# Performance work log

Measured on AMD Instinct MI355X. Metric: run time of the kernel, lower is better.

Reference implementation:

```python
import jax, jax.numpy as jnp
import numpy as np

COST_CLASS, COST_BBOX, COST_GIOU = 1.0, 5.0, 2.0  # init_kwargs weights


def cxcywh_to_xyxy(b):
    cx, cy, w, h = jnp.split(b, 4, axis=-1)
    return jnp.concatenate([cx - 0.5 * w, cy - 0.5 * h, cx + 0.5 * w, cy + 0.5 * h], axis=-1)


def generalized_box_iou(a, b):
    # a: [N,4], b: [M,4], xyxy. Returns [N,M] pairwise GIoU.
    area_a = (a[:, 2] - a[:, 0]) * (a[:, 3] - a[:, 1])
    area_b = (b[:, 2] - b[:, 0]) * (b[:, 3] - b[:, 1])
    lt = jnp.maximum(a[:, None, :2], b[None, :, :2])
    rb = jnp.minimum(a[:, None, 2:], b[None, :, 2:])
    wh = jnp.clip(rb - lt, 0.0)
    inter = wh[..., 0] * wh[..., 1]
    union = area_a[:, None] + area_b[None, :] - inter
    iou = inter / union
    lt_e = jnp.minimum(a[:, None, :2], b[None, :, :2])
    rb_e = jnp.maximum(a[:, None, 2:], b[None, :, 2:])
    wh_e = jnp.clip(rb_e - lt_e, 0.0)
    area_e = wh_e[..., 0] * wh_e[..., 1]
    return iou - (area_e - union) / area_e


def setup_inputs() -> dict:
    key = jax.random.key(0)
    k1, k2, k3, k4 = jax.random.split(key, 4)
    B, Q, C1, T = 16, 900, 257, 128
    pred_logits = jax.random.normal(k1, (B, Q, C1), dtype=jnp.float32)
    pb = jax.random.uniform(k2, (B, Q, 4), dtype=jnp.float32)
    # centers in (0,1), w/h in (0.05, 0.35) so boxes are valid normalized cxcywh
    pred_boxes = jnp.concatenate([pb[..., :2], 0.05 + 0.3 * pb[..., 2:]], axis=-1)
    tb = jax.random.uniform(k3, (B, T, 4), dtype=jnp.float32)
    tgt_boxes = jnp.concatenate([tb[..., :2], 0.05 + 0.3 * tb[..., 2:]], axis=-1)
    tgt_labels = jax.random.randint(k4, (B, T), 0, C1)
    return {"pred_logits": pred_logits, "pred_boxes": pred_boxes,
            "tgt_boxes": tgt_boxes, "tgt_labels": tgt_labels}


def reference(pred_logits, pred_boxes, tgt_boxes, tgt_labels):
    # Faithful to HungarianMatcher.forward up to the scipy linear_sum_assignment
    # (CPU combinatorial step, excluded; see notes). Returns the per-image cost
    # matrices (B, Q, T) that the original feeds to the assignment solver.
    B, Q = pred_logits.shape[:2]
    T = tgt_labels.shape[1]
    probs = jax.nn.softmax(pred_logits.reshape(B * Q, -1), axis=-1)   # (BQ, C+1)
    pboxes = pred_boxes.reshape(B * Q, 4)
    tl = tgt_labels.reshape(-1)                                       # (BT,)
    tb = tgt_boxes.reshape(-1, 4)                                     # (BT, 4)
    cost_class = -probs[:, tl]                                        # (BQ, BT)
    cost_bbox = jnp.sum(jnp.abs(pboxes[:, None, :] - tb[None, :, :]), axis=-1)  # L1 cdist
    cost_giou = -generalized_box_iou(cxcywh_to_xyxy(pboxes), cxcywh_to_xyxy(tb))
    cost = COST_CLASS * cost_class + COST_BBOX * cost_bbox + COST_GIOU * cost_giou
    cost = cost.reshape(B, Q, B, T)
    # original splits the (B, Q, B*T) matrix per image and takes block i of row i
    per_image = cost[jnp.arange(B), :, jnp.arange(B), :]              # (B, Q, T)
    return per_image
```

## Files before the change

### kernel.cpp

```cpp
#include <hip/hip_runtime.h>
#include <math.h>

constexpr int B  = 16;
constexpr int Q  = 900;
constexpr int C1 = 257;
constexpr int T  = 128;

__global__ __launch_bounds__(128) void matcher_kernel(
    const float* __restrict__ logits,
    const float* __restrict__ pboxes,
    const float* __restrict__ tboxes,
    const int*   __restrict__ tlabels,
    float*       __restrict__ out)
{
    const int q   = blockIdx.x;
    const int b   = blockIdx.y;
    const int row = b * Q + q;
    const int tid = threadIdx.x;

    __shared__ float s_exp[C1];
    __shared__ float s_red[2];

    const float* lrow = logits + (size_t)row * C1;
    const float v0 = lrow[tid];
    const float v1 = lrow[tid + 128];
    const float v2 = (tid == 0) ? lrow[256] : -INFINITY;

    float lmax = fmaxf(fmaxf(v0, v1), v2);
    #pragma unroll
    for (int off = 32; off > 0; off >>= 1)
        lmax = fmaxf(lmax, __shfl_down(lmax, off));
    if ((tid & 63) == 0) s_red[tid >> 6] = lmax;
    __syncthreads();
    const float m = fmaxf(s_red[0], s_red[1]);

    const float e0 = __expf(v0 - m);
    const float e1 = __expf(v1 - m);
    s_exp[tid]       = e0;
    s_exp[tid + 128] = e1;
    float lsum = e0 + e1;
    if (tid == 0) {
        const float e2 = __expf(v2 - m);
        s_exp[256] = e2;
        lsum += e2;
    }
    #pragma unroll
    for (int off = 32; off > 0; off >>= 1)
        lsum += __shfl_down(lsum, off);
    __syncthreads();
    if ((tid & 63) == 0) s_red[tid >> 6] = lsum;
    __syncthreads();
    const float invZ = 1.0f / (s_red[0] + s_red[1]);

    const int t     = tid;
    const int label = tlabels[b * T + t];
    const float prob = s_exp[label] * invZ;

    const float4 p  = ((const float4*)pboxes)[row];
    const float4 tb = ((const float4*)tboxes)[b * T + t];

    const float cb = fabsf(p.x - tb.x) + fabsf(p.y - tb.y)
                   + fabsf(p.z - tb.z) + fabsf(p.w - tb.w);

    const float ax0 = p.x - 0.5f * p.z, ay0 = p.y - 0.5f * p.w;
    const float ax1 = p.x + 0.5f * p.z, ay1 = p.y + 0.5f * p.w;
    const float bx0 = tb.x - 0.5f * tb.z, by0 = tb.y - 0.5f * tb.w;
    const float bx1 = tb.x + 0.5f * tb.z, by1 = tb.y + 0.5f * tb.w;

    const float area_a = (ax1 - ax0) * (ay1 - ay0);
    const float area_b = (bx1 - bx0) * (by1 - by0);

    float iw = fminf(ax1, bx1) - fmaxf(ax0, bx0); iw = fmaxf(iw, 0.0f);
    float ih = fminf(ay1, by1) - fmaxf(ay0, by0); ih = fmaxf(ih, 0.0f);
    const float inter = iw * ih;
    const float uni   = area_a + area_b - inter;
    const float iou   = inter / uni;

    float ew = fmaxf(ax1, bx1) - fminf(ax0, bx0); ew = fmaxf(ew, 0.0f);
    float eh = fmaxf(ay1, by1) - fminf(ay0, by0); eh = fmaxf(eh, 0.0f);
    const float area_e = ew * eh;

    const float giou = iou - (area_e - uni) / area_e;

    const float cost = -prob + 5.0f * cb - 2.0f * giou;
    out[(size_t)row * T + t] = cost;
}

extern "C" void kernel_launch(void* const* d_in, const int* in_sizes, int n_in,
                              void* d_out, int out_size, void* d_ws, size_t ws_size,
                              hipStream_t stream) {
    const float* logits  = (const float*)d_in[0];
    const float* pboxes  = (const float*)d_in[1];
    const float* tboxes  = (const float*)d_in[2];
    const int*   tlabels = (const int*)d_in[3];
    float* out = (float*)d_out;

    dim3 grid(Q, B);
    dim3 block(128);
    matcher_kernel<<<grid, block, 0, stream>>>(logits, pboxes, tboxes, tlabels, out);
}
```

Baseline: 74.28 us.

## Process four query rows per block with wave-level softmax and shared target data

After: 72.41 us. -2.5%, faster.

```diff
diff --git a/kernel.cpp b/kernel.cpp
--- a/kernel.cpp
+++ b/kernel.cpp
@@ -5,85 +5,91 @@
 constexpr int Q  = 900;
 constexpr int C1 = 257;
 constexpr int T  = 128;
+constexpr int ROWS_PER_BLOCK = 4;
 
-__global__ __launch_bounds__(128) void matcher_kernel(
+__global__ __launch_bounds__(256) void matcher_kernel(
     const float* __restrict__ logits,
     const float* __restrict__ pboxes,
     const float* __restrict__ tboxes,
     const int*   __restrict__ tlabels,
     float*       __restrict__ out)
 {
-    const int q   = blockIdx.x;
-    const int b   = blockIdx.y;
-    const int row = b * Q + q;
-    const int tid = threadIdx.x;
+    const int tid  = threadIdx.x;
+    const int w    = tid >> 6;
+    const int lane = tid & 63;
+    const int b    = blockIdx.y;
+    const int q    = blockIdx.x * ROWS_PER_BLOCK + w;
+    const int row  = b * Q + q;
 
-    __shared__ float s_exp[C1];
-    __shared__ float s_red[2];
+    __shared__ float s_exp[ROWS_PER_BLOCK][C1 + 3];
+    __shared__ float s_tx0[T], s_ty0[T], s_tx1[T], s_ty1[T], s_tarea[T];
+    __shared__ int   s_lab[T];
+
+    if (tid < T) {
+        const float4 tb = ((const float4*)tboxes)[b * T + tid];
+        const float x0 = tb.x - 0.5f * tb.z, y0 = tb.y - 0.5f * tb.w;
+        const float x1 = tb.x + 0.5f * tb.z, y1 = tb.y + 0.5f * tb.w;
+        s_tx0[tid] = x0; s_ty0[tid] = y0; s_tx1[tid] = x1; s_ty1[tid] = y1;
+        s_tarea[tid] = (x1 - x0) * (y1 - y0);
+        s_lab[tid] = tlabels[b * T + tid];
+    }
 
     const float* lrow = logits + (size_t)row * C1;
-    const float v0 = lrow[tid];
-    const float v1 = lrow[tid + 128];
-    const float v2 = (tid == 0) ? lrow[256] : -INFINITY;
+    const float e0 = __expf(lrow[lane]);
+    const float e1 = __expf(lrow[lane + 64]);
+    const float e2 = __expf(lrow[lane + 128]);
+    const float e3 = __expf(lrow[lane + 192]);
+    float etail = 0.0f;
+    if (lane == 0) etail = __expf(lrow[256]);
 
-    float lmax = fmaxf(fmaxf(v0, v1), v2);
+    s_exp[w][lane]       = e0;
+    s_exp[w][lane + 64]  = e1;
+    s_exp[w][lane + 128] = e2;
+    s_exp[w][lane + 192] = e3;
+    if (lane == 0) s_exp[w][256] = etail;
+
+    float sum = e0 + e1 + e2 + e3 + etail;
     #pragma unroll
     for (int off = 32; off > 0; off >>= 1)
-        lmax = fmaxf(lmax, __shfl_down(lmax, off));
-    if ((tid & 63) == 0) s_red[tid >> 6] = lmax;
-    __syncthreads();
-    const float m = fmaxf(s_red[0], s_red[1]);
-
-    const float e0 = __expf(v0 - m);
-    const float e1 = __expf(v1 - m);
-    s_exp[tid]       = e0;
-    s_exp[tid + 128] = e1;
-    float lsum = e0 + e1;
-    if (tid == 0) {
-        const float e2 = __expf(v2 - m);
-        s_exp[256] = e2;
-        lsum += e2;
-    }
-    #pragma unroll
-    for (int off = 32; off > 0; off >>= 1)
-        lsum += __shfl_down(lsum, off);
-    __syncthreads();
-    if ((tid & 63) == 0) s_red[tid >> 6] = lsum;
-    __syncthreads();
-    const float invZ = 1.0f / (s_red[0] + s_red[1]);
-
-    const int t     = tid;
-    const int label = tlabels[b * T + t];
-    const float prob = s_exp[label] * invZ;
+        sum += __shfl_xor(sum, off);
+    const float invZ = 1.0f / sum;
 
     const float4 p  = ((const float4*)pboxes)[row];
-    const float4 tb = ((const float4*)tboxes)[b * T + t];
-
-    const float cb = fabsf(p.x - tb.x) + fabsf(p.y - tb.y)
-                   + fabsf(p.z - tb.z) + fabsf(p.w - tb.w);
-
     const float ax0 = p.x - 0.5f * p.z, ay0 = p.y - 0.5f * p.w;
     const float ax1 = p.x + 0.5f * p.z, ay1 = p.y + 0.5f * p.w;
-    const float bx0 = tb.x - 0.5f * tb.z, by0 = tb.y - 0.5f * tb.w;
-    const float bx1 = tb.x + 0.5f * tb.z, by1 = tb.y + 0.5f * tb.w;
+    const float area_a = (ax1 - ax0) * (ay1 - ay0);
 
-    const float area_a = (ax1 - ax0) * (ay1 - ay0);
-    const float area_b = (bx1 - bx0) * (by1 - by0);
+    __syncthreads();
 
-    float iw = fminf(ax1, bx1) - fmaxf(ax0, bx0); iw = fmaxf(iw, 0.0f);
-    float ih = fminf(ay1, by1) - fmaxf(ay0, by0); ih = fmaxf(ih, 0.0f);
-    const float inter = iw * ih;
-    const float uni   = area_a + area_b - inter;
-    const float iou   = inter / uni;
+    float* orow = out + (size_t)row * T;
+    #pragma unroll
+    for (int half = 0; half < 2; ++half) {
+        const int t = lane + 64 * half;
+        const float prob = s_exp[w][s_lab[t]] * invZ;
 
-    float ew = fmaxf(ax1, bx1) - fminf(ax0, bx0); ew = fmaxf(ew, 0.0f);
-    float eh = fmaxf(ay1, by1) - fminf(ay0, by0); eh = fmaxf(eh, 0.0f);
-    const float area_e = ew * eh;
+        const float bx0 = s_tx0[t], by0 = s_ty0[t];
+        const float bx1 = s_tx1[t], by1 = s_ty1[t];
+        const float area_b = s_tarea[t];
 
-    const float giou = iou - (area_e - uni) / area_e;
+        const float tcx = 0.5f * (bx0 + bx1), tcy = 0.5f * (by0 + by1);
+        const float tw  = bx1 - bx0,          th  = by1 - by0;
+        const float cb = fabsf(p.x - tcx) + fabsf(p.y - tcy)
+                       + fabsf(p.z - tw)  + fabsf(p.w - th);
 
-    const float cost = -prob + 5.0f * cb - 2.0f * giou;
-    out[(size_t)row * T + t] = cost;
+        float iw = fminf(ax1, bx1) - fmaxf(ax0, bx0); iw = fmaxf(iw, 0.0f);
+        float ih = fminf(ay1, by1) - fmaxf(ay0, by0); ih = fmaxf(ih, 0.0f);
+        const float inter = iw * ih;
+        const float uni   = area_a + area_b - inter;
+        const float iou   = inter / uni;
+
+        float ew = fmaxf(ax1, bx1) - fminf(ax0, bx0);
+        float eh = fmaxf(ay1, by1) - fminf(ay0, by0);
+        const float area_e = ew * eh;
+
+        const float giou = iou - (area_e - uni) / area_e;
+
+        orow[t] = -prob + 5.0f * cb - 2.0f * giou;
+    }
 }
 
 extern "C" void kernel_launch(void* const* d_in, const int* in_sizes, int n_in,
@@ -95,7 +101,7 @@
     const int*   tlabels = (const int*)d_in[3];
     float* out = (float*)d_out;
 
-    dim3 grid(Q, B);
-    dim3 block(128);
+    dim3 grid(Q / ROWS_PER_BLOCK, B);
+    dim3 block(256);
     matcher_kernel<<<grid, block, 0, stream>>>(logits, pboxes, tboxes, tlabels, out);
 }
```
